# Kernel optimization log

Measured on AMD Instinct MI355X. Metric: run time of the kernel, lower is better.

## Reference

```python
import jax, jax.numpy as jnp
import numpy as np

# Standard NF4 quantization levels (bitsandbytes / QLoRA)
NF4_LEVELS = jnp.array([
    -1.0, -0.6961928009986877, -0.5250730514526367, -0.39491748809814453,
    -0.28444138169288635, -0.18477343022823334, -0.09105003625154495, 0.0,
    0.07958029955625534, 0.16093020141124725, 0.24611230194568634,
    0.33791524171829224, 0.44070982933044434, 0.5626170039176941,
    0.7229568362236023, 1.0], dtype=jnp.float32)

D_IN, D_OUT = 4096, 4096
BLOCK_SIZE = 64
N_VALS = D_IN * D_OUT              # 16_777_216 weights
N_BYTES = N_VALS // 2              # 2 nibbles per byte
NUM_BLOCKS = N_VALS // BLOCK_SIZE  # 262_144 per-block scales


def setup_inputs() -> dict:
    key = jax.random.key(0)
    k1, k2, k3, k4 = jax.random.split(key, 4)
    x = jax.random.normal(k1, (4, 2048, D_IN), dtype=jnp.float32)
    kernel_quantized = jax.random.randint(k2, (N_BYTES,), 0, 256, dtype=jnp.int32)
    kernel_scales = jax.random.uniform(k3, (NUM_BLOCKS,), dtype=jnp.float32)
    bias = jax.random.normal(k4, (D_OUT,), dtype=jnp.float32)
    return {"x": x, "kernel_quantized": kernel_quantized,
            "kernel_scales": kernel_scales, "bias": bias}


def nf4_dequantize(kernel_quantized, kernel_scales):
    # Unpack two 4-bit codes per byte (high nibble first), look up NF4 level,
    # scale per block of BLOCK_SIZE values, reshape to original kernel shape.
    high = (kernel_quantized >> 4) & 0xF
    low = kernel_quantized & 0xF
    codes = jnp.stack([high, low], axis=-1).reshape(-1)          # [N_VALS]
    vals = NF4_LEVELS[codes]                                     # [N_VALS]
    vals = vals.reshape(NUM_BLOCKS, BLOCK_SIZE) * kernel_scales[:, None]
    return vals.reshape(D_IN, D_OUT)                             # pad_length = 0


def reference(x, kernel_quantized, kernel_scales, bias):
    # Dense base-layer call on the dequantized kernel: x @ W + b
    W = nf4_dequantize(kernel_quantized, kernel_scales)
    out = jnp.einsum('bsd,de->bse', x, W) + bias
    return out.astype(jnp.float32)
```

## Files before the change

kernel.cpp:

```cpp
#include <hip/hip_runtime.h>
#include <hip/hip_bf16.h>
#include <stdint.h>

typedef __bf16 bf16x8 __attribute__((ext_vector_type(8)));
typedef float f32x16 __attribute__((ext_vector_type(16)));
typedef unsigned short ushort_t;
typedef ushort_t ushort8 __attribute__((ext_vector_type(8)));

#define GLDS16(g, l) __builtin_amdgcn_global_load_lds(                          \
    (const __attribute__((address_space(1))) void*)(g),                         \
    (__attribute__((address_space(3))) void*)(l), 16, 0, 0)

__device__ __constant__ float NF4_LUT_C[16] = {
    -1.0f, -0.6961928009986877f, -0.5250730514526367f, -0.39491748809814453f,
    -0.28444138169288635f, -0.18477343022823334f, -0.09105003625154495f, 0.0f,
    0.07958029955625534f, 0.16093020141124725f, 0.24611230194568634f,
    0.33791524171829224f, 0.44070982933044434f, 0.5626170039176941f,
    0.7229568362236023f, 1.0f};

__device__ inline ushort_t f32_to_bf16(float f) {
    uint32_t u = __builtin_bit_cast(uint32_t, f);
    u += 0x7FFFu + ((u >> 16) & 1u);
    return (ushort_t)(u >> 16);
}


__global__ __launch_bounds__(256) void cast_x_kernel(
    const float* __restrict__ x, ushort_t* __restrict__ A_pk)
{
    __shared__ ushort_t lt[32][130];
    const int t  = threadIdx.x;
    const int mb = blockIdx.x >> 5;
    const int kc = blockIdx.x & 31;

    {
        const int rl = t >> 3;
        const int c0 = (t & 7) * 16;
        const float4* p = reinterpret_cast<const float4*>(
            x + (size_t)(mb * 32 + rl) * 4096 + kc * 128 + c0);
        #pragma unroll
        for (int q = 0; q < 4; ++q) {
            float4 a = p[q];
            lt[rl][c0 + q * 4 + 0] = f32_to_bf16(a.x);
            lt[rl][c0 + q * 4 + 1] = f32_to_bf16(a.y);
            lt[rl][c0 + q * 4 + 2] = f32_to_bf16(a.z);
            lt[rl][c0 + q * 4 + 3] = f32_to_bf16(a.w);
        }
    }
    __syncthreads();

    ushort_t* dst = A_pk + ((size_t)mb * 256 + kc * 8) * 512 + t * 16;
    #pragma unroll
    for (int h = 0; h < 2; ++h) {
        const int c  = 2 * t + h;
        const int kb = c >> 6;
        const int l  = c & 63;
        const int rl = l & 31;
        const int k0 = kb * 16 + (l >> 5) * 8;
        ushort8 v;
        #pragma unroll
        for (int e = 0; e < 8; ++e) v[e] = lt[rl][k0 + e];
        *reinterpret_cast<ushort8*>(dst + h * 8) = v;
    }
}

__global__ __launch_bounds__(256) void nf4_dequant_t_kernel(
    const int* __restrict__ q, const float* __restrict__ scales,
    ushort_t* __restrict__ B_pk)
{
    __shared__ float lut[16];
    __shared__ ushort_t tile[64][65];
    const int t = threadIdx.x;
    if (t < 16) lut[t] = NF4_LUT_C[t];
    __syncthreads();

    const int nt = blockIdx.x & 63;
    const int kt = blockIdx.x >> 6;

    #pragma unroll
    for (int L = t; L < 512; L += 256) {
        const int r  = L >> 3;
        const int qd = L & 7;
        const int k  = kt * 64 + r;
        const int4 e4 = *reinterpret_cast<const int4*>(q + (size_t)k * 2048 + nt * 32 + qd * 4);
        const float s = scales[k * 64 + nt];
        const int nb = qd * 8;
        int bts[4] = {e4.x, e4.y, e4.z, e4.w};
        #pragma unroll
        for (int e = 0; e < 4; ++e) {
            const int byte = bts[e];
            tile[r][nb + e * 2]     = f32_to_bf16(lut[(byte >> 4) & 0xF] * s);
            tile[r][nb + e * 2 + 1] = f32_to_bf16(lut[byte & 0xF] * s);
        }
    }
    __syncthreads();

    #pragma unroll
    for (int h = 0; h < 2; ++h) {
        const int c   = 2 * t + h;
        const int nbl = c >> 8;
        const int kbl = (c >> 6) & 3;
        const int l   = c & 63;
        const int nl  = nbl * 32 + (l & 31);
        const int k0  = kbl * 16 + (l >> 5) * 8;
        ushort8 v;
        #pragma unroll
        for (int e = 0; e < 8; ++e) v[e] = tile[k0 + e][nl];
        ushort_t* dst = B_pk + ((size_t)(nt * 2 + nbl) * 256 + kt * 4 + kbl) * 512 + l * 8;
        *reinterpret_cast<ushort8*>(dst) = v;
    }
}

__global__ __launch_bounds__(512, 2) void gemm_nf4_kernel(
    const ushort_t* __restrict__ A_pk, const ushort_t* __restrict__ B_pk,
    const float* __restrict__ bias, float* __restrict__ C)
{
    __shared__ __align__(16) ushort_t As[2][16384];
    __shared__ __align__(16) ushort_t Bs[2][16384];

    const int tid  = threadIdx.x;
    const int lane = tid & 63;
    const int w8   = tid >> 6;
    const int wr   = w8 >> 2;
    const int wc   = w8 & 3;
    const int ln31 = lane & 31;
    const int lq2  = lane >> 5;

    const int wg  = blockIdx.x;
    const int swz = (wg & 7) * 64 + (wg >> 3);
    const int m0  = (swz >> 4) * 256;
    const int n0  = (swz & 15) * 256;

    const ushort_t* gA = A_pk + ((size_t)(m0 >> 5) + w8) * (256 * 512) + lane * 8;
    const ushort_t* gB = B_pk + ((size_t)(n0 >> 5) + w8) * (256 * 512) + lane * 8;

    f32x16 acc[4][2];
    #pragma unroll
    for (int i = 0; i < 4; ++i)
        #pragma unroll
        for (int j = 0; j < 2; ++j)
            acc[i][j] = (f32x16){0.f};

    const int aBase = wr * 8192 + lane * 8;
    const int bBase = wc * 4096 + lane * 8;

    #pragma unroll
    for (int qq = 0; qq < 4; ++qq) {
        GLDS16(gA + qq * 512, &As[0][(w8 * 4 + qq) * 512]);
        GLDS16(gB + qq * 512, &Bs[0][(w8 * 4 + qq) * 512]);
    }
    asm volatile("s_waitcnt vmcnt(0)" ::: "memory");
    __builtin_amdgcn_s_barrier();
    __builtin_amdgcn_sched_barrier(0);

    for (int t = 0; t < 64; ++t) {
        const int p = t & 1;

        if (t < 63) {
            const int kof = (t + 1) * 2048;
            #pragma unroll
            for (int qq = 0; qq < 4; ++qq) {
                GLDS16(gA + kof + qq * 512, &As[p ^ 1][(w8 * 4 + qq) * 512]);
                GLDS16(gB + kof + qq * 512, &Bs[p ^ 1][(w8 * 4 + qq) * 512]);
            }
        }

        const ushort_t* Ab = &As[p][aBase];
        const ushort_t* Bb = &Bs[p][bBase];
        #pragma unroll
        for (int kk = 0; kk < 4; ++kk) {
            bf16x8 af[4], bf[2];
            #pragma unroll
            for (int i = 0; i < 4; ++i)
                af[i] = *reinterpret_cast<const bf16x8*>(Ab + (i * 4 + kk) * 512);
            #pragma unroll
            for (int j = 0; j < 2; ++j)
                bf[j] = *reinterpret_cast<const bf16x8*>(Bb + (j * 4 + kk) * 512);
            __builtin_amdgcn_s_setprio(1);
            #pragma unroll
            for (int i = 0; i < 4; ++i)
                #pragma unroll
                for (int j = 0; j < 2; ++j)
                    acc[i][j] = __builtin_amdgcn_mfma_f32_32x32x16_bf16(
                        af[i], bf[j], acc[i][j], 0, 0, 0);
            __builtin_amdgcn_s_setprio(0);
        }

        if (t < 63) asm volatile("s_waitcnt vmcnt(0)" ::: "memory");
        __builtin_amdgcn_s_barrier();
        __builtin_amdgcn_sched_barrier(0);
    }

    const int crow_b = m0 + wr * 128 + lq2 * 4;
    const int ccol_b = n0 + wc * 64 + ln31;
    #pragma unroll
    for (int j = 0; j < 2; ++j) {
        const int c = ccol_b + j * 32;
        const float bv = bias[c];
        #pragma unroll
        for (int i = 0; i < 4; ++i) {
            #pragma unroll
            for (int reg = 0; reg < 16; ++reg) {
                const int r = crow_b + i * 32 + (reg & 3) + 8 * (reg >> 2);
                C[(size_t)r * 4096 + c] = acc[i][j][reg] + bv;
            }
        }
    }
}

extern "C" void kernel_launch(void* const* d_in, const int* in_sizes, int n_in,
                              void* d_out, int out_size, void* d_ws, size_t ws_size,
                              hipStream_t stream) {
    const float* x      = (const float*)d_in[0];
    const int*   q      = (const int*)d_in[1];
    const float* scales = (const float*)d_in[2];
    const float* bias   = (const float*)d_in[3];
    float* out = (float*)d_out;

    ushort_t* A_pk = (ushort_t*)d_ws;
    ushort_t* B_pk = (ushort_t*)((char*)d_ws + (size_t)64 * 1024 * 1024);

    cast_x_kernel<<<8192, 256, 0, stream>>>(x, A_pk);
    nf4_dequant_t_kernel<<<4096, 256, 0, stream>>>(q, scales, B_pk);
    gemm_nf4_kernel<<<512, 512, 0, stream>>>(A_pk, B_pk, bias, out);
}
```

Baseline: 317.8 us.

## Use four-stage LDS ring with smaller K tiles and deeper prefetch in GEMM

Replaces the double-buffered K=64 LDS tiles with a 4-slot ring of K=32 tiles, prefetching three tiles ahead. Global-to-LDS loads are split and interleaved between the two MFMA halves, and partial vmcnt waits keep up to eight loads in flight across barriers. This aims to hide memory latency better and avoid the full vmcnt(0) drain every iteration. In exchange it runs twice as many barriers per K.

Result: faster. 303.8 us (-4.4%).

```diff
diff --git a/kernel.cpp b/kernel.cpp
--- a/kernel.cpp
+++ b/kernel.cpp
@@ -115,8 +115,8 @@
     const ushort_t* __restrict__ A_pk, const ushort_t* __restrict__ B_pk,
     const float* __restrict__ bias, float* __restrict__ C)
 {
-    __shared__ __align__(16) ushort_t As[2][16384];
-    __shared__ __align__(16) ushort_t Bs[2][16384];
+    __shared__ __align__(16) ushort_t As[4][8192];
+    __shared__ __align__(16) ushort_t Bs[4][8192];
 
     const int tid  = threadIdx.x;
     const int lane = tid & 63;
@@ -141,52 +141,70 @@
         for (int j = 0; j < 2; ++j)
             acc[i][j] = (f32x16){0.f};
 
-    const int aBase = wr * 8192 + lane * 8;
-    const int bBase = wc * 4096 + lane * 8;
-
-    #pragma unroll
-    for (int qq = 0; qq < 4; ++qq) {
-        GLDS16(gA + qq * 512, &As[0][(w8 * 4 + qq) * 512]);
-        GLDS16(gB + qq * 512, &Bs[0][(w8 * 4 + qq) * 512]);
-    }
-    asm volatile("s_waitcnt vmcnt(0)" ::: "memory");
+    const int aBase = wr * 4096 + lane * 8;
+    const int bBase = wc * 2048 + lane * 8;
+
+    #pragma unroll
+    for (int tt = 0; tt < 3; ++tt) {
+        #pragma unroll
+        for (int kb = 0; kb < 2; ++kb) {
+            GLDS16(gA + (tt * 2 + kb) * 512, &As[tt][(w8 * 2 + kb) * 512]);
+            GLDS16(gB + (tt * 2 + kb) * 512, &Bs[tt][(w8 * 2 + kb) * 512]);
+        }
+    }
+    asm volatile("s_waitcnt vmcnt(8)" ::: "memory");
     __builtin_amdgcn_s_barrier();
     __builtin_amdgcn_sched_barrier(0);
 
-    for (int t = 0; t < 64; ++t) {
-        const int p = t & 1;
-
-        if (t < 63) {
-            const int kof = (t + 1) * 2048;
-            #pragma unroll
-            for (int qq = 0; qq < 4; ++qq) {
-                GLDS16(gA + kof + qq * 512, &As[p ^ 1][(w8 * 4 + qq) * 512]);
-                GLDS16(gB + kof + qq * 512, &Bs[p ^ 1][(w8 * 4 + qq) * 512]);
-            }
-        }
-
-        const ushort_t* Ab = &As[p][aBase];
-        const ushort_t* Bb = &Bs[p][bBase];
-        #pragma unroll
-        for (int kk = 0; kk < 4; ++kk) {
-            bf16x8 af[4], bf[2];
-            #pragma unroll
-            for (int i = 0; i < 4; ++i)
-                af[i] = *reinterpret_cast<const bf16x8*>(Ab + (i * 4 + kk) * 512);
+    for (int t = 0; t < 128; ++t) {
+        const int slot  = t & 3;
+        const int nslot = (t + 3) & 3;
+        const ushort_t* Asl = &As[slot][aBase];
+        const ushort_t* Bsl = &Bs[slot][bBase];
+        const int kof = (t + 3) * 1024;
+
+        bf16x8 af0[4], bf0[2], af1[4], bf1[2];
+        #pragma unroll
+        for (int i = 0; i < 4; ++i)
+            af0[i] = *reinterpret_cast<const bf16x8*>(Asl + i * 1024);
+        #pragma unroll
+        for (int j = 0; j < 2; ++j)
+            bf0[j] = *reinterpret_cast<const bf16x8*>(Bsl + j * 1024);
+        if (t < 125) {
+            GLDS16(gA + kof,       &As[nslot][(w8 * 2) * 512]);
+            GLDS16(gA + kof + 512, &As[nslot][(w8 * 2 + 1) * 512]);
+        }
+        __builtin_amdgcn_s_setprio(1);
+        #pragma unroll
+        for (int i = 0; i < 4; ++i)
             #pragma unroll
             for (int j = 0; j < 2; ++j)
-                bf[j] = *reinterpret_cast<const bf16x8*>(Bb + (j * 4 + kk) * 512);
-            __builtin_amdgcn_s_setprio(1);
+                acc[i][j] = __builtin_amdgcn_mfma_f32_32x32x16_bf16(
+                    af0[i], bf0[j], acc[i][j], 0, 0, 0);
+        __builtin_amdgcn_s_setprio(0);
+
+        #pragma unroll
+        for (int i = 0; i < 4; ++i)
+            af1[i] = *reinterpret_cast<const bf16x8*>(Asl + i * 1024 + 512);
+        #pragma unroll
+        for (int j = 0; j < 2; ++j)
+            bf1[j] = *reinterpret_cast<const bf16x8*>(Bsl + j * 1024 + 512);
+        if (t < 125) {
+            GLDS16(gB + kof,       &Bs[nslot][(w8 * 2) * 512]);
+            GLDS16(gB + kof + 512, &Bs[nslot][(w8 * 2 + 1) * 512]);
+        }
+        __builtin_amdgcn_s_setprio(1);
+        #pragma unroll
+        for (int i = 0; i < 4; ++i)
             #pragma unroll
-            for (int i = 0; i < 4; ++i)
-                #pragma unroll
-                for (int j = 0; j < 2; ++j)
-                    acc[i][j] = __builtin_amdgcn_mfma_f32_32x32x16_bf16(
-                        af[i], bf[j], acc[i][j], 0, 0, 0);
-            __builtin_amdgcn_s_setprio(0);
-        }
-
-        if (t < 63) asm volatile("s_waitcnt vmcnt(0)" ::: "memory");
+            for (int j = 0; j < 2; ++j)
+                acc[i][j] = __builtin_amdgcn_mfma_f32_32x32x16_bf16(
+                    af1[i], bf1[j], acc[i][j], 0, 0, 0);
+        __builtin_amdgcn_s_setprio(0);
+
+        if (t < 125)       asm volatile("s_waitcnt vmcnt(8)" ::: "memory");
+        else if (t == 125) asm volatile("s_waitcnt vmcnt(4)" ::: "memory");
+        else if (t == 126) asm volatile("s_waitcnt vmcnt(0)" ::: "memory");
         __builtin_amdgcn_s_barrier();
         __builtin_amdgcn_sched_barrier(0);
     }
```

## Split GEMM k-step into four sub-phases with staggered half-tile prefetch

Applied to the files above, without the earlier changes.

Restructures the GEMM main loop into four MFMA phases, each over a quarter of the output sub-tiles. Global-to-LDS loads for the next tiles are issued in halves between phases, so a buffer region is refilled as soon as its last reader finishes, with partial vmcnt waits in place of full drains. The aim is to overlap global memory latency with MFMA work and avoid the per-iteration stall. It adds more barriers per iteration and depends on subtle buffer-reuse ordering being correct.

Result: no change. 317.4 us (-0.1%).

```diff
diff --git a/kernel.cpp b/kernel.cpp
--- a/kernel.cpp
+++ b/kernel.cpp
@@ -111,6 +111,27 @@
     }
 }
 
+#define SYNC_BEFORE_MFMA() do {                                                 \
+    __builtin_amdgcn_sched_barrier(0);                                          \
+    __builtin_amdgcn_s_barrier();                                               \
+    asm volatile("s_waitcnt lgkmcnt(0)" ::: "memory");                          \
+    __builtin_amdgcn_sched_barrier(0);                                          \
+} while (0)
+
+#define CLOSE_PHASE() do {                                                      \
+    __builtin_amdgcn_sched_barrier(0);                                          \
+    __builtin_amdgcn_s_barrier();                                               \
+} while (0)
+
+#define STAGE_A(p_, kt_, b0_, b1_) do {                                         \
+    GLDS16(aCB + (size_t)(b0_) * 131072 + (kt_) * 2048, &As[p_][(b0_) * 2048 + dOff]); \
+    GLDS16(aCB + (size_t)(b1_) * 131072 + (kt_) * 2048, &As[p_][(b1_) * 2048 + dOff]); \
+} while (0)
+#define STAGE_B(p_, kt_, b0_, b1_) do {                                         \
+    GLDS16(bCB + (size_t)(b0_) * 131072 + (kt_) * 2048, &Bs[p_][(b0_) * 2048 + dOff]); \
+    GLDS16(bCB + (size_t)(b1_) * 131072 + (kt_) * 2048, &Bs[p_][(b1_) * 2048 + dOff]); \
+} while (0)
+
 __global__ __launch_bounds__(512, 2) void gemm_nf4_kernel(
     const ushort_t* __restrict__ A_pk, const ushort_t* __restrict__ B_pk,
     const float* __restrict__ bias, float* __restrict__ C)
@@ -131,8 +152,15 @@
     const int m0  = (swz >> 4) * 256;
     const int n0  = (swz & 15) * 256;
 
-    const ushort_t* gA = A_pk + ((size_t)(m0 >> 5) + w8) * (256 * 512) + lane * 8;
-    const ushort_t* gB = B_pk + ((size_t)(n0 >> 5) + w8) * (256 * 512) + lane * 8;
+    const int iA   = tid >> 8;
+    const int kbl  = (tid >> 6) & 3;
+    const int dOff = kbl * 512 + (tid & 63) * 8;
+    const int Ae0 = iA,         Ae1 = 4 + iA;
+    const int Ao0 = 2 + iA,     Ao1 = 6 + iA;
+    const int Be0 = 2 * iA,     Be1 = 4 + 2 * iA;
+    const int Bo0 = 2 * iA + 1, Bo1 = 5 + 2 * iA;
+    const ushort_t* aCB = A_pk + (size_t)(m0 >> 5) * 131072 + kbl * 512 + (tid & 63) * 8;
+    const ushort_t* bCB = B_pk + (size_t)(n0 >> 5) * 131072 + kbl * 512 + (tid & 63) * 8;
 
     f32x16 acc[4][2];
     #pragma unroll
@@ -141,54 +169,92 @@
         for (int j = 0; j < 2; ++j)
             acc[i][j] = (f32x16){0.f};
 
-    const int aBase = wr * 8192 + lane * 8;
-    const int bBase = wc * 4096 + lane * 8;
-
-    #pragma unroll
-    for (int qq = 0; qq < 4; ++qq) {
-        GLDS16(gA + qq * 512, &As[0][(w8 * 4 + qq) * 512]);
-        GLDS16(gB + qq * 512, &Bs[0][(w8 * 4 + qq) * 512]);
-    }
-    asm volatile("s_waitcnt vmcnt(0)" ::: "memory");
+    const int aOff = wr * 8192 + lane * 8;
+    const int bOff = wc * 4096 + lane * 8;
+
+    STAGE_A(0, 0, Ae0, Ae1); STAGE_A(0, 0, Ao0, Ao1);
+    STAGE_B(0, 0, Be0, Be1); STAGE_B(0, 0, Bo0, Bo1);
+    STAGE_A(1, 1, Ae0, Ae1);
+    STAGE_B(1, 1, Be0, Be1); STAGE_B(1, 1, Bo0, Bo1);
+    asm volatile("s_waitcnt vmcnt(6)" ::: "memory");
     __builtin_amdgcn_s_barrier();
     __builtin_amdgcn_sched_barrier(0);
 
-    for (int t = 0; t < 64; ++t) {
-        const int p = t & 1;
-
-        if (t < 63) {
-            const int kof = (t + 1) * 2048;
-            #pragma unroll
-            for (int qq = 0; qq < 4; ++qq) {
-                GLDS16(gA + kof + qq * 512, &As[p ^ 1][(w8 * 4 + qq) * 512]);
-                GLDS16(gB + kof + qq * 512, &Bs[p ^ 1][(w8 * 4 + qq) * 512]);
-            }
-        }
-
-        const ushort_t* Ab = &As[p][aBase];
-        const ushort_t* Bb = &Bs[p][bBase];
-        #pragma unroll
-        for (int kk = 0; kk < 4; ++kk) {
-            bf16x8 af[4], bf[2];
-            #pragma unroll
-            for (int i = 0; i < 4; ++i)
-                af[i] = *reinterpret_cast<const bf16x8*>(Ab + (i * 4 + kk) * 512);
-            #pragma unroll
-            for (int j = 0; j < 2; ++j)
-                bf[j] = *reinterpret_cast<const bf16x8*>(Bb + (j * 4 + kk) * 512);
-            __builtin_amdgcn_s_setprio(1);
-            #pragma unroll
-            for (int i = 0; i < 4; ++i)
-                #pragma unroll
-                for (int j = 0; j < 2; ++j)
-                    acc[i][j] = __builtin_amdgcn_mfma_f32_32x32x16_bf16(
-                        af[i], bf[j], acc[i][j], 0, 0, 0);
-            __builtin_amdgcn_s_setprio(0);
-        }
-
-        if (t < 63) asm volatile("s_waitcnt vmcnt(0)" ::: "memory");
-        __builtin_amdgcn_s_barrier();
-        __builtin_amdgcn_sched_barrier(0);
+    for (int kt = 0; kt < 64; ++kt) {
+        const int p = kt & 1;
+        const ushort_t* Ab = &As[p][aOff];
+        const ushort_t* Bb = &Bs[p][bOff];
+
+        bf16x8 af[2][4], bf0[4], bf1[4];
+
+        #pragma unroll
+        for (int i = 0; i < 2; ++i)
+            #pragma unroll
+            for (int kk = 0; kk < 4; ++kk)
+                af[i][kk] = *reinterpret_cast<const bf16x8*>(Ab + i * 2048 + kk * 512);
+        #pragma unroll
+        for (int kk = 0; kk < 4; ++kk)
+            bf0[kk] = *reinterpret_cast<const bf16x8*>(Bb + kk * 512);
+        if (kt < 63) STAGE_A(p ^ 1, kt + 1, Ao0, Ao1);
+        SYNC_BEFORE_MFMA();
+        __builtin_amdgcn_s_setprio(1);
+        #pragma unroll
+        for (int i = 0; i < 2; ++i)
+            #pragma unroll
+            for (int kk = 0; kk < 4; ++kk)
+                acc[i][0] = __builtin_amdgcn_mfma_f32_32x32x16_bf16(
+                    af[i][kk], bf0[kk], acc[i][0], 0, 0, 0);
+        __builtin_amdgcn_s_setprio(0);
+        CLOSE_PHASE();
+
+        #pragma unroll
+        for (int kk = 0; kk < 4; ++kk)
+            bf1[kk] = *reinterpret_cast<const bf16x8*>(Bb + 2048 + kk * 512);
+        if (kt < 62) STAGE_A(p, kt + 2, Ae0, Ae1);
+        SYNC_BEFORE_MFMA();
+        __builtin_amdgcn_s_setprio(1);
+        #pragma unroll
+        for (int i = 0; i < 2; ++i)
+            #pragma unroll
+            for (int kk = 0; kk < 4; ++kk)
+                acc[i][1] = __builtin_amdgcn_mfma_f32_32x32x16_bf16(
+                    af[i][kk], bf1[kk], acc[i][1], 0, 0, 0);
+        __builtin_amdgcn_s_setprio(0);
+        CLOSE_PHASE();
+
+        #pragma unroll
+        for (int i = 0; i < 2; ++i)
+            #pragma unroll
+            for (int kk = 0; kk < 4; ++kk)
+                af[i][kk] = *reinterpret_cast<const bf16x8*>(Ab + (2 + i) * 2048 + kk * 512);
+        if (kt < 62) STAGE_B(p, kt + 2, Be0, Be1);
+        SYNC_BEFORE_MFMA();
+        __builtin_amdgcn_s_setprio(1);
+        #pragma unroll
+        for (int i = 0; i < 2; ++i)
+            #pragma unroll
+            for (int kk = 0; kk < 4; ++kk)
+                acc[2 + i][0] = __builtin_amdgcn_mfma_f32_32x32x16_bf16(
+                    af[i][kk], bf0[kk], acc[2 + i][0], 0, 0, 0);
+        __builtin_amdgcn_s_setprio(0);
+        CLOSE_PHASE();
+
+        if (kt < 62) {
+            STAGE_B(p, kt + 2, Bo0, Bo1);
+            asm volatile("s_waitcnt vmcnt(6)" ::: "memory");
+        } else if (kt == 62) {
+            asm volatile("s_waitcnt vmcnt(0)" ::: "memory");
+        }
+        SYNC_BEFORE_MFMA();
+        __builtin_amdgcn_s_setprio(1);
+        #pragma unroll
+        for (int i = 0; i < 2; ++i)
+            #pragma unroll
+            for (int kk = 0; kk < 4; ++kk)
+                acc[2 + i][1] = __builtin_amdgcn_mfma_f32_32x32x16_bf16(
+                    af[i][kk], bf1[kk], acc[2 + i][1], 0, 0, 0);
+        __builtin_amdgcn_s_setprio(0);
+        CLOSE_PHASE();
     }
 
     const int crow_b = m0 + wr * 128 + lq2 * 4;
```
